# Optimization experiments

Measured on AMD Instinct MI355X. Metric: run time of the kernel, lower is better.

## Reference

```python
import jax, jax.numpy as jnp
import numpy as np

THRESH = 0.5
DECAY = 0.2
D_IN = 784
H1 = 2048
H2 = 10
K = 10
U = D_IN + H1
L = 128
B = 1024


def setup_inputs() -> dict:
    key = jax.random.key(0)
    ks = jax.random.split(key, 6)
    inp = jax.random.uniform(ks[0], (B, D_IN), dtype=jnp.float32)
    W1 = jax.random.normal(ks[1], (H1, D_IN), dtype=jnp.float32) * 0.05
    b1 = jnp.zeros((H1,), dtype=jnp.float32)
    W2 = jax.random.normal(ks[2], (H2, H1), dtype=jnp.float32) * 0.05
    b2 = jnp.zeros((H2,), dtype=jnp.float32)
    # core_mem_all[k][u][0] -> sparse-ish per-unit vector, [1] -> count
    core_mem_vec = (jax.random.uniform(ks[3], (K, U, L)) > 0.7).astype(jnp.float32)
    core_mem_cnt = jax.random.randint(ks[4], (K, U), 0, 5).astype(jnp.int32)
    return {"input": inp, "W1": W1, "b1": b1, "W2": W2, "b2": b2,
            "core_mem_vec": core_mem_vec, "core_mem_cnt": core_mem_cnt,
            "time_window": 20}


def act_fun(mem):
    # spike = Heaviside(mem - thresh)
    return (mem > THRESH).astype(mem.dtype)


def reference(input, W1, b1, W2, b2, core_mem_vec, core_mem_cnt, time_window):
    batch, d_in = input.shape
    h1 = W1.shape[0]
    h2 = W2.shape[0]
    Lv = core_mem_vec.shape[-1]

    # Precompute, per (core k, unit u): contribution to count_add_1 / count_add_2
    # when unit u spikes. count_add_1 += (last nonzero index of temp) - 1 when cnt>0;
    # count_add_2 += cnt when cnt>0. Sum over cores up front (loop order irrelevant).
    nz = core_mem_vec != 0                                     # [K,U,L]
    has = nz.any(-1)
    last_idx = Lv - 1 - jnp.argmax(nz[..., ::-1].astype(jnp.int32), axis=-1)  # [K,U]
    active = (core_mem_cnt > 0) & has
    val1 = jnp.where(active, last_idx - 1, 0).sum(0).astype(jnp.float32)      # [U]
    val2 = jnp.where(core_mem_cnt > 0, core_mem_cnt, 0).sum(0).astype(jnp.float32)
    v1x, v1h = val1[:d_in], val1[d_in:]
    v2x, v2h = val2[:d_in], val2[d_in:]

    key = jax.random.key(42)

    def step(carry, t):
        h1m, h1s, h2m, h2s, h2sum, a1, a2, cs = carry
        # Bernoulli rate encoding of the input image
        x = (input > jax.random.uniform(jax.random.fold_in(key, t), input.shape)).astype(jnp.float32)
        # mem_update: mem = mem*decay*(1-spike) + W x + b ; spike = mem > thresh
        h1m = h1m * DECAY * (1.0 - h1s) + x @ W1.T + b1
        h1s = act_fun(h1m)
        h2m = h2m * DECAY * (1.0 - h2s) + h1s @ W2.T + b2
        h2s = act_fun(h2m)
        h2sum = h2sum + h2s
        # vectorized core-memory gather/count: sum per-unit precomputed values
        # over all spiking units, across the batch
        xs = x.sum(0)      # [784] spike counts per input unit this step
        hs = h1s.sum(0)    # [h1]
        a1 = a1 + xs @ v1x + hs @ v1h
        a2 = a2 + xs @ v2x + hs @ v2h
        cs = cs + xs.sum() + hs.sum()
        return (h1m, h1s, h2m, h2s, h2sum, a1, a2, cs), None

    z1 = jnp.zeros((batch, h1), dtype=jnp.float32)
    z2 = jnp.zeros((batch, h2), dtype=jnp.float32)
    carry = (z1, z1, z2, z2, z2, jnp.float32(0), jnp.float32(0), jnp.float32(0))
    carry, _ = jax.lax.scan(step, carry, jnp.arange(time_window))
    _, _, _, _, h2sum, a1, a2, cs = carry
    outputs = h2sum / time_window
    return outputs, a1, a2, cs
```

## Files before the change

kernel.cpp:

```cpp
#include <hip/hip_runtime.h>
#include <cstdint>
#include <cstddef>

static constexpr int D_IN = 784;
static constexpr int H1   = 2048;
static constexpr int H2   = 10;
static constexpr int KK   = 10;
static constexpr int UU   = 2832;
static constexpr int LL   = 128;
static constexpr int BB   = 1024;
static constexpr int TT   = 20;
static constexpr int HALF = BB * D_IN / 2;
static constexpr int NCH  = 25;
static constexpr int NLIMB = 3;
static constexpr int XA_T  = 32 * NCH * 64;
static constexpr int BITS_T = BB * 64;
static constexpr int PANEL = NCH * NLIMB * 64;
static constexpr int PANEL_PAD = PANEL + 2 * NLIMB * 64;
static constexpr int NPART_GEN = 2000;
static constexpr int NPART_H1  = 256;
static constexpr int NPART = NPART_GEN + NPART_H1;

static constexpr int BLK_VALS  = (KK * UU) / 4;
static constexpr int BLK_W2T   = H1 / 256;
static constexpr int BLK_LIMBS = (64 * NCH * 64) / 256;
static constexpr int BLK_TRANS = D_IN * 4;
static constexpr int SETUP_BLOCKS = BLK_VALS + BLK_W2T + BLK_LIMBS + BLK_TRANS;

typedef int v4i  __attribute__((ext_vector_type(4)));
typedef int v16i __attribute__((ext_vector_type(16)));

#define MFMA_I8 __builtin_amdgcn_mfma_i32_32x32x32_i8

__device__ __forceinline__ uint32_t rotl32(uint32_t x, int d) {
  return (x << d) | (x >> (32 - d));
}
__device__ __forceinline__ void threefry2x32(uint32_t k0, uint32_t k1,
                                             uint32_t& x0, uint32_t& x1) {
  uint32_t ks2 = k0 ^ k1 ^ 0x1BD11BDAu;
  x0 += k0; x1 += k1;
#define TF_R(r) { x0 += x1; x1 = rotl32(x1, (r)); x1 ^= x0; }
  TF_R(13) TF_R(15) TF_R(26) TF_R(6)
  x0 += k1;  x1 += ks2 + 1u;
  TF_R(17) TF_R(29) TF_R(16) TF_R(24)
  x0 += ks2; x1 += k0 + 2u;
  TF_R(13) TF_R(15) TF_R(26) TF_R(6)
  x0 += k0;  x1 += k1 + 3u;
  TF_R(17) TF_R(29) TF_R(16) TF_R(24)
  x0 += k1;  x1 += ks2 + 4u;
  TF_R(13) TF_R(15) TF_R(26) TF_R(6)
  x0 += ks2; x1 += k0 + 5u;
#undef TF_R
}
__device__ __forceinline__ float bits_to_unif(uint32_t b) {
  uint32_t fb = (b >> 9) | 0x3F800000u;
  return __uint_as_float(fb) - 1.0f;
}

__device__ __forceinline__ double wave_red(double v) {
  #pragma unroll
  for (int off = 32; off > 0; off >>= 1) v += __shfl_down(v, off, 64);
  return v;
}
__device__ __forceinline__ void block_store3(double s0, double s1, double s2,
                                             double* slot) {
  __shared__ double lds[3][8];
  int lane = threadIdx.x & 63, w = threadIdx.x >> 6;
  int nw = (int)(blockDim.x >> 6);
  s0 = wave_red(s0); s1 = wave_red(s1); s2 = wave_red(s2);
  if (lane == 0) { lds[0][w] = s0; lds[1][w] = s1; lds[2][w] = s2; }
  __syncthreads();
  if (threadIdx.x == 0) {
    double t0 = 0, t1 = 0, t2 = 0;
    for (int i = 0; i < nw; i++) { t0 += lds[0][i]; t1 += lds[1][i]; t2 += lds[2][i]; }
    slot[0] = t0; slot[1] = t1; slot[2] = t2;
  }
}

__global__ __launch_bounds__(256)
void setup(const float* __restrict__ cmv, const int* __restrict__ cmc,
           float* __restrict__ v1, float* __restrict__ v2,
           const float* __restrict__ W2, float* __restrict__ W2T,
           const float* __restrict__ W1, v4i* __restrict__ W1L,
           const float* __restrict__ input, float* __restrict__ inT) {
  int bx = blockIdx.x;
  if (bx < BLK_VALS) {
    int gw = (bx * 256 + threadIdx.x) >> 6;
    int lane = threadIdx.x & 63;
    const float* p = cmv + (size_t)gw * LL;
    float a = p[lane];
    float b = p[lane + 64];
    unsigned long long mlo = __ballot(a != 0.0f);
    unsigned long long mhi = __ballot(b != 0.0f);
    if (lane == 0) {
      int u = gw % UU;
      int c = cmc[gw];
      int last = mhi ? (127 - __builtin_clzll(mhi))
                     : (mlo ? (63 - __builtin_clzll(mlo)) : -1);
      if (c > 0) {
        if (last >= 0) atomicAdd(&v1[u], (float)(last - 1));
        atomicAdd(&v2[u], (float)c);
      }
    }
  } else if (bx < BLK_VALS + BLK_W2T) {
    int i = (bx - BLK_VALS) * 256 + threadIdx.x;
    #pragma unroll
    for (int j = 0; j < H2; j++) W2T[i * H2 + j] = W2[j * H1 + i];
  } else if (bx < BLK_VALS + BLK_W2T + BLK_LIMBS) {
    int tid = (bx - BLK_VALS - BLK_W2T) * 256 + threadIdx.x;
    int lane = tid & 63;
    int tc = tid >> 6;
    int n = ((tc / NCH) << 5) + (lane & 31);
    int chunk = tc % NCH;
    int k0 = chunk * 32 + (lane >> 5) * 16;
    union { v4i v; signed char b[16]; } d[NLIMB];
    #pragma unroll
    for (int j = 0; j < 16; j++) {
      long long F = 0;
      int k = k0 + j;
      if (k < D_IN) {
        double w = (double)W1[(size_t)n * D_IN + k];
        F = llround(w * 0x1p24);
        if (F >  8355711LL) F =  8355711LL;
        if (F < -8421504LL) F = -8421504LL;
      }
      #pragma unroll
      for (int l = 0; l < NLIMB; l++) {
        int dig = (int)((F + 128) & 255) - 128;
        d[l].b[j] = (signed char)dig;
        F = (F - dig) >> 8;
      }
    }
    #pragma unroll
    for (int l = 0; l < NLIMB; l++) W1L[(size_t)(tc * NLIMB + l) * 64 + lane] = d[l].v;
  } else {
    int b = bx - (BLK_VALS + BLK_W2T + BLK_LIMBS);
    int k = b >> 2;
    int m = ((b & 3) << 8) + threadIdx.x;
    inT[(size_t)k * BB + m] = input[(size_t)m * D_IN + k];
  }
}

__global__ __launch_bounds__(256)
void gen_all(const float* __restrict__ inT, v4i* __restrict__ XA,
             const float* __restrict__ v1, const float* __restrict__ v2,
             double* __restrict__ gpart) {
  int t  = blockIdx.x / 100;
  int gw = (blockIdx.x % 100) * 4 + (threadIdx.x >> 6);
  int lane = threadIdx.x & 63;
  int mtile = gw / NCH, chunk = gw - mtile * NCH;
  int m = (mtile << 5) + (lane & 31);
  int k0 = chunk * 32 + (lane >> 5) * 16;
  uint32_t f0 = 0u, f1 = (uint32_t)t;
  threefry2x32(0u, 42u, f0, f1);
  union { v4i v; unsigned char b[16]; } r0, r1;
  double s0 = 0, s1 = 0, s2 = 0;
  v4i* XA_t = XA + (size_t)t * XA_T;
  if (k0 < D_IN) {
    #pragma unroll
    for (int j = 0; j < 16; j++) {
      int k = k0 + j;
      uint32_t c0 = (uint32_t)(m * D_IN + k), c1 = c0 + (uint32_t)HALF;
      threefry2x32(f0, f1, c0, c1);
      float u0 = bits_to_unif(c0), u1 = bits_to_unif(c1);
      float i0 = inT[(size_t)k * BB + m];
      float i1 = inT[(size_t)k * BB + m + 512];
      unsigned char x0 = (i0 > u0) ? 1 : 0;
      unsigned char x1 = (i1 > u1) ? 1 : 0;
      r0.b[j] = x0; r1.b[j] = x1;
      double xsum = (double)(x0 + x1);
      s0 += xsum * (double)v1[k];
      s1 += xsum * (double)v2[k];
      s2 += xsum;
    }
  } else {
    r0.v = (v4i){0, 0, 0, 0};
    r1.v = (v4i){0, 0, 0, 0};
  }
  XA_t[(size_t)(mtile * NCH + chunk) * 64 + lane] = r0.v;
  XA_t[(size_t)((mtile + 16) * NCH + chunk) * 64 + lane] = r1.v;
  block_store3(s0, s1, s2, gpart + 3 * (size_t)blockIdx.x);
}

__global__ __launch_bounds__(512)
void h1_all(const v4i* __restrict__ XA, const v4i* __restrict__ W1L,
            const float* __restrict__ b1, uint32_t* __restrict__ bits,
            const float* __restrict__ v1, const float* __restrict__ v2,
            double* __restrict__ gpart) {
  extern __shared__ v4i bl[];
  int lane = threadIdx.x & 63, wv = threadIdx.x >> 6;
  int id = blockIdx.x + (blockIdx.y << 6);
  int xcd = id & 7;
  int idx = id >> 3;
  int ntile = (idx << 1) | (xcd >> 2);
  int mtg = xcd & 3;
  int mt = mtg * 8 + wv;
  {
    const v4i* wp = W1L + (size_t)ntile * PANEL;
    for (int i = threadIdx.x; i < PANEL; i += 512) bl[i] = wp[i];
  }
  __syncthreads();

  int col = lane & 31;
  int gn = (ntile << 5) + col;
  float bias = b1[gn];
  double v1n = (double)v1[D_IN + gn], v2n = (double)v2[D_IN + gn];
  int scnt = 0;
  float mreg[16];
  #pragma unroll
  for (int r = 0; r < 16; r++) mreg[r] = 0.0f;

  const v4i* bq = bl + lane;
  #pragma unroll 1
  for (int tp = 0; tp < TT / 2; tp++) {
    const v4i* a0 = XA + (size_t)(2 * tp) * XA_T + (size_t)mt * (NCH * 64) + lane;
    const v4i* a1 = a0 + XA_T;
    v16i c00 = {}, c01 = {}, c02 = {};
    v16i c10 = {}, c11 = {}, c12 = {};
    v4i A0c = a0[0],   A1c = a1[0];
    v4i A0n = a0[64],  A1n = a1[64];
    v4i A0m = a0[128], A1m = a1[128];
    v4i B0c = bq[0],   B1c = bq[64],  B2c = bq[128];
    v4i B0n = bq[192], B1n = bq[256], B2n = bq[320];
    #pragma unroll 1
    for (int c = 0; c < NCH; c++) {
      v4i A0f = a0[(c + 3) * 64], A1f = a1[(c + 3) * 64];
      const v4i* br = bq + (size_t)(c + 2) * (NLIMB * 64);
      v4i B0f = br[0], B1f = br[64], B2f = br[128];
      c00 = MFMA_I8(A0c, B0c, c00, 0, 0, 0);
      c10 = MFMA_I8(A1c, B0c, c10, 0, 0, 0);
      c01 = MFMA_I8(A0c, B1c, c01, 0, 0, 0);
      c11 = MFMA_I8(A1c, B1c, c11, 0, 0, 0);
      c02 = MFMA_I8(A0c, B2c, c02, 0, 0, 0);
      c12 = MFMA_I8(A1c, B2c, c12, 0, 0, 0);
      A0c = A0n; A1c = A1n; A0n = A0m; A1n = A1m; A0m = A0f; A1m = A1f;
      B0c = B0n; B1c = B1n; B2c = B2n; B0n = B0f; B1n = B1f; B2n = B2f;
    }
    #pragma unroll
    for (int half = 0; half < 2; half++) {
      const v16i& q0 = half ? c10 : c00;
      const v16i& q1 = half ? c11 : c01;
      const v16i& q2 = half ? c12 : c02;
      uint32_t* btm = bits + (size_t)(2 * tp + half) * BITS_T
                    + ((size_t)mt << 5) * 64 + ntile;
      #pragma unroll
      for (int r = 0; r < 16; r++) {
        int val = (int)((uint32_t)q0[r] + ((uint32_t)q1[r] << 8)
                        + ((uint32_t)q2[r] << 16));
        float dot = (float)val * 0x1p-24f + bias;
        float mp = mreg[r];
        float mnew = (mp > 0.5f) ? dot : fmaf(mp, 0.2f, dot);
        bool s = (mnew > 0.5f);
        mreg[r] = mnew;
        unsigned long long bm = __ballot(s);
        int rowA = (r & 3) + 8 * (r >> 2);
        if ((lane & 31) == 0)
          btm[(size_t)(rowA + ((lane >> 5) << 2)) * 64] = (uint32_t)(bm >> (lane & 32));
        scnt += s ? 1 : 0;
      }
    }
  }
  double sc = (double)scnt;
  block_store3(sc * v1n, sc * v2n, sc, gpart + 3 * (size_t)(NPART_GEN + id));
}

__global__ __launch_bounds__(256)
void h2_all(const uint32_t* __restrict__ bits, const float* __restrict__ W2T,
            const float* __restrict__ b2, const double* __restrict__ gpart,
            float* __restrict__ out) {
  int lane = threadIdx.x & 63, wq = threadIdx.x >> 6;
  int b0 = blockIdx.x * 2;
  float w[8][10];
  #pragma unroll
  for (int c = 0; c < 8; c++) {
    int n = (wq << 9) + (c << 6) + lane;
    #pragma unroll
    for (int j = 0; j < 10; j++) w[c][j] = W2T[(size_t)n * H2 + j];
  }
  float m = 0.0f, sp = 0.0f, sm = 0.0f;
  float b2v = (lane < 10) ? b2[lane] : 0.0f;
  __shared__ float part[4][2][10];
  #pragma unroll 1
  for (int t = 0; t < TT; t++) {
    const uint32_t* bt = bits + (size_t)t * BITS_T;
    #pragma unroll
    for (int r = 0; r < 2; r++) {
      uint32_t myw = bt[(size_t)(b0 + r) * 64 + (wq << 4) + (lane & 15)];
      float p[10];
      #pragma unroll
      for (int j = 0; j < 10; j++) p[j] = 0.0f;
      #pragma unroll
      for (int c = 0; c < 8; c++) {
        uint32_t wd = __shfl(myw, (c << 1) + (lane >> 5), 64);
        float f = (float)((wd >> (lane & 31)) & 1u);
        #pragma unroll
        for (int j = 0; j < 10; j++) p[j] += f * w[c][j];
      }
      #pragma unroll
      for (int j = 0; j < 10; j++) {
        float v = p[j];
        #pragma unroll
        for (int off = 32; off > 0; off >>= 1) v += __shfl_xor(v, off, 64);
        p[j] = v;
      }
      if (lane == 0) {
        #pragma unroll
        for (int j = 0; j < 10; j++) part[wq][r][j] = p[j];
      }
    }
    __syncthreads();
    if (wq < 2 && lane < 10) {
      float red = part[0][wq][lane] + part[1][wq][lane]
                + part[2][wq][lane] + part[3][wq][lane];
      m = m * 0.2f * (1.0f - sp) + red + b2v;
      sp = (m > 0.5f) ? 1.0f : 0.0f;
      sm += sp;
    }
    __syncthreads();
  }
  if (wq < 2 && lane < 10)
    out[(size_t)(b0 + wq) * H2 + lane] = (float)((double)sm / (double)TT);

  if (blockIdx.x == 0) {
    double t0 = 0, t1 = 0, t2 = 0;
    for (int i = threadIdx.x; i < NPART; i += 256) {
      t0 += gpart[3 * (size_t)i];
      t1 += gpart[3 * (size_t)i + 1];
      t2 += gpart[3 * (size_t)i + 2];
    }
    __shared__ double fin[3][4];
    t0 = wave_red(t0); t1 = wave_red(t1); t2 = wave_red(t2);
    if (lane == 0) { fin[0][wq] = t0; fin[1][wq] = t1; fin[2][wq] = t2; }
    __syncthreads();
    if (threadIdx.x == 0) {
      double a = 0, b = 0, cc = 0;
      #pragma unroll
      for (int i = 0; i < 4; i++) { a += fin[0][i]; b += fin[1][i]; cc += fin[2][i]; }
      out[(size_t)BB * H2 + 0] = (float)a;
      out[(size_t)BB * H2 + 1] = (float)b;
      out[(size_t)BB * H2 + 2] = (float)cc;
    }
  }
}

extern "C" void kernel_launch(void* const* d_in, const int* in_sizes, int n_in,
                              void* d_out, int out_size, void* d_ws, size_t ws_size,
                              hipStream_t stream) {
  (void)in_sizes; (void)n_in; (void)out_size; (void)ws_size;
  const float* input = (const float*)d_in[0];
  const float* W1    = (const float*)d_in[1];
  const float* b1    = (const float*)d_in[2];
  const float* W2    = (const float*)d_in[3];
  const float* b2    = (const float*)d_in[4];
  const float* cmv   = (const float*)d_in[5];
  const int*   cmc   = (const int*)d_in[6];

  char* base = (char*)d_ws;
  float*  v1   = (float*)(base + 0);
  float*  v2   = (float*)(base + 11328);
  const size_t ZERO_BYTES = 22656;
  float*  W2T  = (float*)(base + 22656);
  v4i*    W1L  = (v4i*)(base + 104576);
  v4i*    XA   = (v4i*)(base + 5019776);
  uint32_t* bits = (uint32_t*)(base + 21407872);
  float*  inT  = (float*)(base + 26650752);
  double* gpart = (double*)(base + 29862016);

  hipMemsetAsync(d_ws, 0, ZERO_BYTES, stream);

  setup<<<SETUP_BLOCKS, 256, 0, stream>>>(cmv, cmc, v1, v2, W2, W2T, W1, W1L,
                                          input, inT);
  gen_all<<<TT * 100, 256, 0, stream>>>(inT, XA, v1, v2, gpart);
  h1_all<<<dim3(64, 4), 512, PANEL_PAD * 16, stream>>>(XA, W1L, b1, bits, v1, v2,
                                                       gpart);
  h2_all<<<BB / 2, 256, 0, stream>>>(bits, W2T, b2, gpart, (float*)d_out);
}
```

Before: 320.1 us.

## Fuse spike generation into setup kernel and defer input-count reduction

Merges the input transpose, setup and Bernoulli spike generation into one prep kernel. The generator now reads input rows directly with float4 loads, so the transposed copy goes away. It counts spikes per input unit with ballot/popcount and integer atomics into a zeroed buffer, so the v1/v2-weighted sums are done once in h2_all. The h1 MFMA loop drops manual software prefetch for a fully unrolled loop with setprio and launch_bounds(512,2). This saves one launch, the transposed buffer traffic and per-block double reductions, at the cost of atomic contention and of leaving load scheduling to the compiler.

```diff
diff --git a/kernel.cpp b/kernel.cpp
--- a/kernel.cpp
+++ b/kernel.cpp
@@ -16,16 +16,13 @@
 static constexpr int XA_T  = 32 * NCH * 64;
 static constexpr int BITS_T = BB * 64;
 static constexpr int PANEL = NCH * NLIMB * 64;
-static constexpr int PANEL_PAD = PANEL + 2 * NLIMB * 64;
-static constexpr int NPART_GEN = 2000;
-static constexpr int NPART_H1  = 256;
-static constexpr int NPART = NPART_GEN + NPART_H1;
+static constexpr int NPART = 256;
 
 static constexpr int BLK_VALS  = (KK * UU) / 4;
 static constexpr int BLK_W2T   = H1 / 256;
 static constexpr int BLK_LIMBS = (64 * NCH * 64) / 256;
-static constexpr int BLK_TRANS = D_IN * 4;
-static constexpr int SETUP_BLOCKS = BLK_VALS + BLK_W2T + BLK_LIMBS + BLK_TRANS;
+static constexpr int BLK_GEN   = TT * 100;
+static constexpr int PREP_BLOCKS = BLK_VALS + BLK_W2T + BLK_LIMBS + BLK_GEN;
 
 typedef int v4i  __attribute__((ext_vector_type(4)));
 typedef int v16i __attribute__((ext_vector_type(16)));
@@ -78,11 +75,12 @@
 }
 
 __global__ __launch_bounds__(256)
-void setup(const float* __restrict__ cmv, const int* __restrict__ cmc,
-           float* __restrict__ v1, float* __restrict__ v2,
-           const float* __restrict__ W2, float* __restrict__ W2T,
-           const float* __restrict__ W1, v4i* __restrict__ W1L,
-           const float* __restrict__ input, float* __restrict__ inT) {
+void prep(const float* __restrict__ cmv, const int* __restrict__ cmc,
+          float* __restrict__ v1, float* __restrict__ v2,
+          const float* __restrict__ W2, float* __restrict__ W2T,
+          const float* __restrict__ W1, v4i* __restrict__ W1L,
+          const float* __restrict__ input, v4i* __restrict__ XA,
+          int* __restrict__ xcnt) {
   int bx = blockIdx.x;
   if (bx < BLK_VALS) {
     int gw = (bx * 256 + threadIdx.x) >> 6;
@@ -134,55 +132,59 @@
     #pragma unroll
     for (int l = 0; l < NLIMB; l++) W1L[(size_t)(tc * NLIMB + l) * 64 + lane] = d[l].v;
   } else {
-    int b = bx - (BLK_VALS + BLK_W2T + BLK_LIMBS);
-    int k = b >> 2;
-    int m = ((b & 3) << 8) + threadIdx.x;
-    inT[(size_t)k * BB + m] = input[(size_t)m * D_IN + k];
-  }
-}
-
-__global__ __launch_bounds__(256)
-void gen_all(const float* __restrict__ inT, v4i* __restrict__ XA,
-             const float* __restrict__ v1, const float* __restrict__ v2,
-             double* __restrict__ gpart) {
-  int t  = blockIdx.x / 100;
-  int gw = (blockIdx.x % 100) * 4 + (threadIdx.x >> 6);
-  int lane = threadIdx.x & 63;
-  int mtile = gw / NCH, chunk = gw - mtile * NCH;
-  int m = (mtile << 5) + (lane & 31);
-  int k0 = chunk * 32 + (lane >> 5) * 16;
-  uint32_t f0 = 0u, f1 = (uint32_t)t;
-  threefry2x32(0u, 42u, f0, f1);
-  union { v4i v; unsigned char b[16]; } r0, r1;
-  double s0 = 0, s1 = 0, s2 = 0;
-  v4i* XA_t = XA + (size_t)t * XA_T;
-  if (k0 < D_IN) {
-    #pragma unroll
-    for (int j = 0; j < 16; j++) {
-      int k = k0 + j;
-      uint32_t c0 = (uint32_t)(m * D_IN + k), c1 = c0 + (uint32_t)HALF;
-      threefry2x32(f0, f1, c0, c1);
-      float u0 = bits_to_unif(c0), u1 = bits_to_unif(c1);
-      float i0 = inT[(size_t)k * BB + m];
-      float i1 = inT[(size_t)k * BB + m + 512];
-      unsigned char x0 = (i0 > u0) ? 1 : 0;
-      unsigned char x1 = (i1 > u1) ? 1 : 0;
-      r0.b[j] = x0; r1.b[j] = x1;
-      double xsum = (double)(x0 + x1);
-      s0 += xsum * (double)v1[k];
-      s1 += xsum * (double)v2[k];
-      s2 += xsum;
-    }
-  } else {
-    r0.v = (v4i){0, 0, 0, 0};
-    r1.v = (v4i){0, 0, 0, 0};
-  }
-  XA_t[(size_t)(mtile * NCH + chunk) * 64 + lane] = r0.v;
-  XA_t[(size_t)((mtile + 16) * NCH + chunk) * 64 + lane] = r1.v;
-  block_store3(s0, s1, s2, gpart + 3 * (size_t)blockIdx.x);
-}
-
-__global__ __launch_bounds__(512)
+    int gb = bx - (BLK_VALS + BLK_W2T + BLK_LIMBS);
+    int t  = gb / 100;
+    int gw = (gb % 100) * 4 + (threadIdx.x >> 6);
+    int lane = threadIdx.x & 63;
+    int mtile = gw / NCH, chunk = gw - mtile * NCH;
+    int m = (mtile << 5) + (lane & 31);
+    int k0 = chunk * 32 + (lane >> 5) * 16;
+    uint32_t f0 = 0u, f1 = (uint32_t)t;
+    threefry2x32(0u, 42u, f0, f1);
+    union { v4i v; unsigned char b[16]; } r0, r1;
+    v4i* XA_t = XA + (size_t)t * XA_T;
+    if (k0 < D_IN) {
+      const float4* I0 = (const float4*)(input + (size_t)m * D_IN + k0);
+      const float4* I1 = (const float4*)(input + (size_t)(m + 512) * D_IN + k0);
+      float i0v[16], i1v[16];
+      #pragma unroll
+      for (int q = 0; q < 4; q++) {
+        float4 a = I0[q], b4 = I1[q];
+        i0v[q * 4 + 0] = a.x;  i0v[q * 4 + 1] = a.y;
+        i0v[q * 4 + 2] = a.z;  i0v[q * 4 + 3] = a.w;
+        i1v[q * 4 + 0] = b4.x; i1v[q * 4 + 1] = b4.y;
+        i1v[q * 4 + 2] = b4.z; i1v[q * 4 + 3] = b4.w;
+      }
+      int cnt[16];
+      #pragma unroll
+      for (int j = 0; j < 16; j++) {
+        int k = k0 + j;
+        uint32_t c0 = (uint32_t)(m * D_IN + k), c1 = c0 + (uint32_t)HALF;
+        threefry2x32(f0, f1, c0, c1);
+        float u0 = bits_to_unif(c0), u1 = bits_to_unif(c1);
+        unsigned char x0 = (i0v[j] > u0) ? 1 : 0;
+        unsigned char x1 = (i1v[j] > u1) ? 1 : 0;
+        r0.b[j] = x0; r1.b[j] = x1;
+        unsigned long long b0 = __ballot(x0 != 0);
+        unsigned long long b1 = __ballot(x1 != 0);
+        cnt[j] = (lane < 32)
+               ? (__popc((uint32_t)b0) + __popc((uint32_t)b1))
+               : (__popc((uint32_t)(b0 >> 32)) + __popc((uint32_t)(b1 >> 32)));
+      }
+      if ((lane & 31) == 0) {
+        #pragma unroll
+        for (int j = 0; j < 16; j++) atomicAdd(&xcnt[k0 + j], cnt[j]);
+      }
+    } else {
+      r0.v = (v4i){0, 0, 0, 0};
+      r1.v = (v4i){0, 0, 0, 0};
+    }
+    XA_t[(size_t)(mtile * NCH + chunk) * 64 + lane] = r0.v;
+    XA_t[(size_t)((mtile + 16) * NCH + chunk) * 64 + lane] = r1.v;
+  }
+}
+
+__global__ __launch_bounds__(512, 2)
 void h1_all(const v4i* __restrict__ XA, const v4i* __restrict__ W1L,
             const float* __restrict__ b1, uint32_t* __restrict__ bits,
             const float* __restrict__ v1, const float* __restrict__ v2,
@@ -217,25 +219,20 @@
     const v4i* a1 = a0 + XA_T;
     v16i c00 = {}, c01 = {}, c02 = {};
     v16i c10 = {}, c11 = {}, c12 = {};
-    v4i A0c = a0[0],   A1c = a1[0];
-    v4i A0n = a0[64],  A1n = a1[64];
-    v4i A0m = a0[128], A1m = a1[128];
-    v4i B0c = bq[0],   B1c = bq[64],  B2c = bq[128];
-    v4i B0n = bq[192], B1n = bq[256], B2n = bq[320];
-    #pragma unroll 1
+    __builtin_amdgcn_s_setprio(1);
+    #pragma unroll
     for (int c = 0; c < NCH; c++) {
-      v4i A0f = a0[(c + 3) * 64], A1f = a1[(c + 3) * 64];
-      const v4i* br = bq + (size_t)(c + 2) * (NLIMB * 64);
-      v4i B0f = br[0], B1f = br[64], B2f = br[128];
-      c00 = MFMA_I8(A0c, B0c, c00, 0, 0, 0);
-      c10 = MFMA_I8(A1c, B0c, c10, 0, 0, 0);
-      c01 = MFMA_I8(A0c, B1c, c01, 0, 0, 0);
-      c11 = MFMA_I8(A1c, B1c, c11, 0, 0, 0);
-      c02 = MFMA_I8(A0c, B2c, c02, 0, 0, 0);
-      c12 = MFMA_I8(A1c, B2c, c12, 0, 0, 0);
-      A0c = A0n; A1c = A1n; A0n = A0m; A1n = A1m; A0m = A0f; A1m = A1f;
-      B0c = B0n; B1c = B1n; B2c = B2n; B0n = B0f; B1n = B1f; B2n = B2f;
-    }
+      v4i A0 = a0[c * 64], A1 = a1[c * 64];
+      const v4i* br = bq + (size_t)c * (NLIMB * 64);
+      v4i B0 = br[0], B1 = br[64], B2 = br[128];
+      c00 = MFMA_I8(A0, B0, c00, 0, 0, 0);
+      c10 = MFMA_I8(A1, B0, c10, 0, 0, 0);
+      c01 = MFMA_I8(A0, B1, c01, 0, 0, 0);
+      c11 = MFMA_I8(A1, B1, c11, 0, 0, 0);
+      c02 = MFMA_I8(A0, B2, c02, 0, 0, 0);
+      c12 = MFMA_I8(A1, B2, c12, 0, 0, 0);
+    }
+    __builtin_amdgcn_s_setprio(0);
     #pragma unroll
     for (int half = 0; half < 2; half++) {
       const v16i& q0 = half ? c10 : c00;
@@ -261,13 +258,14 @@
     }
   }
   double sc = (double)scnt;
-  block_store3(sc * v1n, sc * v2n, sc, gpart + 3 * (size_t)(NPART_GEN + id));
+  block_store3(sc * v1n, sc * v2n, sc, gpart + 3 * (size_t)id);
 }
 
 __global__ __launch_bounds__(256)
 void h2_all(const uint32_t* __restrict__ bits, const float* __restrict__ W2T,
             const float* __restrict__ b2, const double* __restrict__ gpart,
-            float* __restrict__ out) {
+            const int* __restrict__ xcnt, const float* __restrict__ v1,
+            const float* __restrict__ v2, float* __restrict__ out) {
   int lane = threadIdx.x & 63, wq = threadIdx.x >> 6;
   int b0 = blockIdx.x * 2;
   float w[8][10];
@@ -327,6 +325,12 @@
       t0 += gpart[3 * (size_t)i];
       t1 += gpart[3 * (size_t)i + 1];
       t2 += gpart[3 * (size_t)i + 2];
+    }
+    for (int k = threadIdx.x; k < D_IN; k += 256) {
+      double c = (double)xcnt[k];
+      t0 += c * (double)v1[k];
+      t1 += c * (double)v2[k];
+      t2 += c;
     }
     __shared__ double fin[3][4];
     t0 = wave_red(t0); t1 = wave_red(t1); t2 = wave_red(t2);
@@ -358,20 +362,20 @@
   char* base = (char*)d_ws;
   float*  v1   = (float*)(base + 0);
   float*  v2   = (float*)(base + 11328);
-  const size_t ZERO_BYTES = 22656;
-  float*  W2T  = (float*)(base + 22656);
-  v4i*    W1L  = (v4i*)(base + 104576);
-  v4i*    XA   = (v4i*)(base + 5019776);
-  uint32_t* bits = (uint32_t*)(base + 21407872);
-  float*  inT  = (float*)(base + 26650752);
-  double* gpart = (double*)(base + 29862016);
+  int*    xcnt = (int*)(base + 22656);
+  const size_t ZERO_BYTES = 25856;
+  float*  W2T  = (float*)(base + 25856);
+  v4i*    W1L  = (v4i*)(base + 107776);
+  v4i*    XA   = (v4i*)(base + 5022976);
+  uint32_t* bits = (uint32_t*)(base + 21406976);
+  double* gpart = (double*)(base + 26649856);
 
   hipMemsetAsync(d_ws, 0, ZERO_BYTES, stream);
 
-  setup<<<SETUP_BLOCKS, 256, 0, stream>>>(cmv, cmc, v1, v2, W2, W2T, W1, W1L,
-                                          input, inT);
-  gen_all<<<TT * 100, 256, 0, stream>>>(inT, XA, v1, v2, gpart);
-  h1_all<<<dim3(64, 4), 512, PANEL_PAD * 16, stream>>>(XA, W1L, b1, bits, v1, v2,
-                                                       gpart);
-  h2_all<<<BB / 2, 256, 0, stream>>>(bits, W2T, b2, gpart, (float*)d_out);
-}
+  prep<<<PREP_BLOCKS, 256, 0, stream>>>(cmv, cmc, v1, v2, W2, W2T, W1, W1L,
+                                        input, XA, xcnt);
+  h1_all<<<dim3(64, 4), 512, PANEL * 16, stream>>>(XA, W1L, b1, bits, v1, v2,
+                                                   gpart);
+  h2_all<<<BB / 2, 256, 0, stream>>>(bits, W2T, b2, gpart, xcnt, v1, v2,
+                                     (float*)d_out);
+}
```

Measured after the change: 383.9 us. 19.9% more time.

## Drop memset with per-unit core reduction; fully unroll h1 MFMA loop with priority

Applied to the files above, without the earlier changes.

The setup pass now has one wave loop over all K cores for a unit and write v1/v2 directly. This removes the atomics and the workspace memset launch. In h1_all the chunk loop is fully unrolled, with the first two chunks of the next time pair prefetched across iterations and s_setprio raised around the MFMA block. A launch-bounds occupancy hint and a smaller LDS allocation are added, which brings register-pressure and spill risk.

```diff
diff --git a/kernel.cpp b/kernel.cpp
--- a/kernel.cpp
+++ b/kernel.cpp
@@ -16,12 +16,11 @@
 static constexpr int XA_T  = 32 * NCH * 64;
 static constexpr int BITS_T = BB * 64;
 static constexpr int PANEL = NCH * NLIMB * 64;
-static constexpr int PANEL_PAD = PANEL + 2 * NLIMB * 64;
 static constexpr int NPART_GEN = 2000;
 static constexpr int NPART_H1  = 256;
 static constexpr int NPART = NPART_GEN + NPART_H1;
 
-static constexpr int BLK_VALS  = (KK * UU) / 4;
+static constexpr int BLK_VALS  = UU / 4;
 static constexpr int BLK_W2T   = H1 / 256;
 static constexpr int BLK_LIMBS = (64 * NCH * 64) / 256;
 static constexpr int BLK_TRANS = D_IN * 4;
@@ -85,23 +84,24 @@
            const float* __restrict__ input, float* __restrict__ inT) {
   int bx = blockIdx.x;
   if (bx < BLK_VALS) {
-    int gw = (bx * 256 + threadIdx.x) >> 6;
+    int u = bx * 4 + (threadIdx.x >> 6);
     int lane = threadIdx.x & 63;
-    const float* p = cmv + (size_t)gw * LL;
-    float a = p[lane];
-    float b = p[lane + 64];
-    unsigned long long mlo = __ballot(a != 0.0f);
-    unsigned long long mhi = __ballot(b != 0.0f);
-    if (lane == 0) {
-      int u = gw % UU;
-      int c = cmc[gw];
-      int last = mhi ? (127 - __builtin_clzll(mhi))
-                     : (mlo ? (63 - __builtin_clzll(mlo)) : -1);
+    float acc1 = 0.0f, acc2 = 0.0f;
+    for (int k = 0; k < KK; k++) {
+      const float* p = cmv + ((size_t)k * UU + u) * LL;
+      float a = p[lane];
+      float b = p[lane + 64];
+      unsigned long long mlo = __ballot(a != 0.0f);
+      unsigned long long mhi = __ballot(b != 0.0f);
+      int c = cmc[k * UU + u];
       if (c > 0) {
-        if (last >= 0) atomicAdd(&v1[u], (float)(last - 1));
-        atomicAdd(&v2[u], (float)c);
-      }
-    }
+        int last = mhi ? (127 - __builtin_clzll(mhi))
+                       : (mlo ? (63 - __builtin_clzll(mlo)) : -1);
+        if (last >= 0) acc1 += (float)(last - 1);
+        acc2 += (float)c;
+      }
+    }
+    if (lane == 0) { v1[u] = acc1; v2[u] = acc2; }
   } else if (bx < BLK_VALS + BLK_W2T) {
     int i = (bx - BLK_VALS) * 256 + threadIdx.x;
     #pragma unroll
@@ -182,7 +182,7 @@
   block_store3(s0, s1, s2, gpart + 3 * (size_t)blockIdx.x);
 }
 
-__global__ __launch_bounds__(512)
+__global__ __launch_bounds__(512, 2)
 void h1_all(const v4i* __restrict__ XA, const v4i* __restrict__ W1L,
             const float* __restrict__ b1, uint32_t* __restrict__ bits,
             const float* __restrict__ v1, const float* __restrict__ v2,
@@ -211,30 +211,47 @@
   for (int r = 0; r < 16; r++) mreg[r] = 0.0f;
 
   const v4i* bq = bl + lane;
+  v4i B00 = bq[0],   B01 = bq[64],  B02 = bq[128];
+  v4i B10 = bq[192], B11 = bq[256], B12 = bq[320];
+  const v4i* a0 = XA + (size_t)mt * (NCH * 64) + lane;
+  const v4i* a1 = a0 + XA_T;
+  v4i A00 = a0[0], A10 = a1[0], A01 = a0[64], A11 = a1[64];
+
   #pragma unroll 1
   for (int tp = 0; tp < TT / 2; tp++) {
-    const v4i* a0 = XA + (size_t)(2 * tp) * XA_T + (size_t)mt * (NCH * 64) + lane;
-    const v4i* a1 = a0 + XA_T;
     v16i c00 = {}, c01 = {}, c02 = {};
     v16i c10 = {}, c11 = {}, c12 = {};
-    v4i A0c = a0[0],   A1c = a1[0];
-    v4i A0n = a0[64],  A1n = a1[64];
-    v4i A0m = a0[128], A1m = a1[128];
-    v4i B0c = bq[0],   B1c = bq[64],  B2c = bq[128];
-    v4i B0n = bq[192], B1n = bq[256], B2n = bq[320];
-    #pragma unroll 1
-    for (int c = 0; c < NCH; c++) {
-      v4i A0f = a0[(c + 3) * 64], A1f = a1[(c + 3) * 64];
-      const v4i* br = bq + (size_t)(c + 2) * (NLIMB * 64);
-      v4i B0f = br[0], B1f = br[64], B2f = br[128];
-      c00 = MFMA_I8(A0c, B0c, c00, 0, 0, 0);
-      c10 = MFMA_I8(A1c, B0c, c10, 0, 0, 0);
-      c01 = MFMA_I8(A0c, B1c, c01, 0, 0, 0);
-      c11 = MFMA_I8(A1c, B1c, c11, 0, 0, 0);
-      c02 = MFMA_I8(A0c, B2c, c02, 0, 0, 0);
-      c12 = MFMA_I8(A1c, B2c, c12, 0, 0, 0);
-      A0c = A0n; A1c = A1n; A0n = A0m; A1n = A1m; A0m = A0f; A1m = A1f;
-      B0c = B0n; B1c = B1n; B2c = B2n; B0n = B0f; B1n = B1f; B2n = B2f;
+    __builtin_amdgcn_s_setprio(1);
+    c00 = MFMA_I8(A00, B00, c00, 0, 0, 0);
+    c10 = MFMA_I8(A10, B00, c10, 0, 0, 0);
+    c01 = MFMA_I8(A00, B01, c01, 0, 0, 0);
+    c11 = MFMA_I8(A10, B01, c11, 0, 0, 0);
+    c02 = MFMA_I8(A00, B02, c02, 0, 0, 0);
+    c12 = MFMA_I8(A10, B02, c12, 0, 0, 0);
+    c00 = MFMA_I8(A01, B10, c00, 0, 0, 0);
+    c10 = MFMA_I8(A11, B10, c10, 0, 0, 0);
+    c01 = MFMA_I8(A01, B11, c01, 0, 0, 0);
+    c11 = MFMA_I8(A11, B11, c11, 0, 0, 0);
+    c02 = MFMA_I8(A01, B12, c02, 0, 0, 0);
+    c12 = MFMA_I8(A11, B12, c12, 0, 0, 0);
+    #pragma unroll
+    for (int c = 2; c < NCH; c++) {
+      v4i A0 = a0[c * 64], A1 = a1[c * 64];
+      const v4i* br = bq + (size_t)c * (NLIMB * 64);
+      v4i B0 = br[0], B1 = br[64], B2 = br[128];
+      c00 = MFMA_I8(A0, B0, c00, 0, 0, 0);
+      c10 = MFMA_I8(A1, B0, c10, 0, 0, 0);
+      c01 = MFMA_I8(A0, B1, c01, 0, 0, 0);
+      c11 = MFMA_I8(A1, B1, c11, 0, 0, 0);
+      c02 = MFMA_I8(A0, B2, c02, 0, 0, 0);
+      c12 = MFMA_I8(A1, B2, c12, 0, 0, 0);
+    }
+    __builtin_amdgcn_s_setprio(0);
+    {
+      const v4i* a0n = a0 + ((tp + 1 < TT / 2) ? 2 * XA_T : 0);
+      const v4i* a1n = a0n + XA_T;
+      A00 = a0n[0]; A10 = a1n[0]; A01 = a0n[64]; A11 = a1n[64];
+      a0 = a0n; a1 = a1n;
     }
     #pragma unroll
     for (int half = 0; half < 2; half++) {
@@ -358,20 +375,17 @@
   char* base = (char*)d_ws;
   float*  v1   = (float*)(base + 0);
   float*  v2   = (float*)(base + 11328);
-  const size_t ZERO_BYTES = 22656;
   float*  W2T  = (float*)(base + 22656);
   v4i*    W1L  = (v4i*)(base + 104576);
   v4i*    XA   = (v4i*)(base + 5019776);
-  uint32_t* bits = (uint32_t*)(base + 21407872);
-  float*  inT  = (float*)(base + 26650752);
-  double* gpart = (double*)(base + 29862016);
-
-  hipMemsetAsync(d_ws, 0, ZERO_BYTES, stream);
+  uint32_t* bits = (uint32_t*)(base + 21403776);
+  float*  inT  = (float*)(base + 26646656);
+  double* gpart = (double*)(base + 29857920);
 
   setup<<<SETUP_BLOCKS, 256, 0, stream>>>(cmv, cmc, v1, v2, W2, W2T, W1, W1L,
                                           input, inT);
   gen_all<<<TT * 100, 256, 0, stream>>>(inT, XA, v1, v2, gpart);
-  h1_all<<<dim3(64, 4), 512, PANEL_PAD * 16, stream>>>(XA, W1L, b1, bits, v1, v2,
-                                                       gpart);
+  h1_all<<<dim3(64, 4), 512, PANEL * 16, stream>>>(XA, W1L, b1, bits, v1, v2,
+                                                   gpart);
   h2_all<<<BB / 2, 256, 0, stream>>>(bits, W2T, b2, gpart, (float*)d_out);
 }
```

Measured after the change: 285.8 us. 1.12x faster.
